# Kernel tuning notes

Measured on AMD Instinct MI355X. Metric: run time of the kernel, lower is better.

Reference implementation:

```python
import jax, jax.numpy as jnp
import numpy as np

MIN_VARIANCE = 0.1
W_MEAN = 1.0
W_DIST = 1.0
W_DISP = 1.0


def setup_inputs() -> dict:
    key = jax.random.key(0)
    k1, k2 = jax.random.split(key)
    cluster1 = jax.random.normal(k1, (8192, 128), dtype=jnp.float32)
    cluster2 = jax.random.normal(k2, (8192, 128), dtype=jnp.float32)
    return {"cluster1": cluster1, "cluster2": cluster2}


def _mean_loss(c1, c2):
    m1 = jnp.mean(c1, axis=0)
    m2 = jnp.mean(c2, axis=0)
    return jnp.mean((m1 - m2) ** 2)  # F.mse_loss default 'mean'


def _distance_loss(c1, c2):
    # min_j ||c1_i - c2_j||^2, fused via ||a||^2 - 2 a b^T + ||b||^2
    sq1 = jnp.sum(c1 * c1, axis=1)  # [N1]
    sq2 = jnp.sum(c2 * c2, axis=1)  # [N2]
    cross = c1 @ c2.T               # [N1, N2]
    d2 = sq1[:, None] - 2.0 * cross + sq2[None, :]
    return jnp.mean(jnp.min(d2, axis=1))


def _dispersion_loss(c, min_variance=MIN_VARIANCE):
    mean = jnp.mean(c, axis=0)
    variances = jnp.mean((c - mean) ** 2, axis=0)
    return jnp.mean(jax.nn.relu(min_variance - variances))


def reference(cluster1, cluster2):
    return (W_MEAN * _mean_loss(cluster1, cluster2)
            + W_DIST * _distance_loss(cluster1, cluster2)
            + W_DISP * _dispersion_loss(cluster1))
```

## Files before the change

kernel.cpp:

```cpp
#include <hip/hip_runtime.h>
#include <hip/hip_bf16.h>

#define N_ROWS 8192
#define DIMS   128

typedef __bf16 bf16x8 __attribute__((ext_vector_type(8)));
typedef float  f32x4  __attribute__((ext_vector_type(4)));

__device__ __forceinline__ unsigned enc_f32(float f) {
    int i = __float_as_int(f);
    return (unsigned)(i ^ ((i >> 31) | 0x80000000));
}
__device__ __forceinline__ float dec_f32(unsigned u) {
    int i = (u & 0x80000000u) ? (int)(u ^ 0x80000000u) : ~(int)u;
    return __int_as_float(i);
}

struct alignas(8) B4 { __hip_bfloat16 h0, h1, h2, h3; };

__global__ __launch_bounds__(256) void prep_k(const float* __restrict__ c1,
                                              const float* __restrict__ c2,
                                              __hip_bfloat16* __restrict__ c1b,
                                              __hip_bfloat16* __restrict__ c2b,
                                              float* __restrict__ sq1,
                                              float* __restrict__ sq2,
                                              float* __restrict__ part,
                                              unsigned* __restrict__ minrow) {
    const int tid  = threadIdx.x;
    const int lane = tid & 63;
    const int wave = tid >> 6;
    const int half = lane >> 5;
    const int l32  = lane & 31;
    const int cl   = blockIdx.x >> 7;
    const int blk  = blockIdx.x & 127;

    if (tid < 32) minrow[blockIdx.x * 32 + tid] = 0xFFFFFFFFu;

    const float* __restrict__ src    = cl ? c2 : c1;
    __hip_bfloat16* __restrict__ dst = cl ? c2b : c1b;
    float* __restrict__ sq           = cl ? sq2 : sq1;
    const float scale                = cl ? 1.0f : -2.0f;

    float4 cs = {0.f, 0.f, 0.f, 0.f};
    float4 cq = {0.f, 0.f, 0.f, 0.f};

    #pragma unroll 4
    for (int i = 0; i < 8; ++i) {
        const int row = blk * 64 + wave * 16 + i * 2 + half;
        float4 x = *reinterpret_cast<const float4*>(src + (size_t)row * DIMS + l32 * 4);
        B4 b4{__float2bfloat16(scale * x.x), __float2bfloat16(scale * x.y),
              __float2bfloat16(scale * x.z), __float2bfloat16(scale * x.w)};
        *reinterpret_cast<B4*>(dst + (size_t)row * DIMS + l32 * 4) = b4;
        float s = x.x * x.x + x.y * x.y + x.z * x.z + x.w * x.w;
        #pragma unroll
        for (int m = 16; m; m >>= 1) s += __shfl_xor(s, m);
        if (l32 == 0) sq[row] = s;
        cs.x += x.x; cs.y += x.y; cs.z += x.z; cs.w += x.w;
        cq.x += x.x * x.x; cq.y += x.y * x.y; cq.z += x.z * x.z; cq.w += x.w * x.w;
    }

    cs.x += __shfl_xor(cs.x, 32); cs.y += __shfl_xor(cs.y, 32);
    cs.z += __shfl_xor(cs.z, 32); cs.w += __shfl_xor(cs.w, 32);
    cq.x += __shfl_xor(cq.x, 32); cq.y += __shfl_xor(cq.y, 32);
    cq.z += __shfl_xor(cq.z, 32); cq.w += __shfl_xor(cq.w, 32);

    __shared__ float4 lds4[4][32];
    lds4[wave][l32] = cs;
    __syncthreads();
    if (tid < 32) {
        float4 a = lds4[0][tid], b = lds4[1][tid], c = lds4[2][tid], d = lds4[3][tid];
        float4 t = {a.x + b.x + c.x + d.x, a.y + b.y + c.y + d.y,
                    a.z + b.z + c.z + d.z, a.w + b.w + c.w + d.w};
        const int base = cl ? 32768 : 0;
        part[base + (4 * tid + 0) * 128 + blk] = t.x;
        part[base + (4 * tid + 1) * 128 + blk] = t.y;
        part[base + (4 * tid + 2) * 128 + blk] = t.z;
        part[base + (4 * tid + 3) * 128 + blk] = t.w;
    }
    __syncthreads();
    lds4[wave][l32] = cq;
    __syncthreads();
    if (tid < 32 && cl == 0) {
        float4 a = lds4[0][tid], b = lds4[1][tid], c = lds4[2][tid], d = lds4[3][tid];
        float4 t = {a.x + b.x + c.x + d.x, a.y + b.y + c.y + d.y,
                    a.z + b.z + c.z + d.z, a.w + b.w + c.w + d.w};
        part[16384 + (4 * tid + 0) * 128 + blk] = t.x;
        part[16384 + (4 * tid + 1) * 128 + blk] = t.y;
        part[16384 + (4 * tid + 2) * 128 + blk] = t.z;
        part[16384 + (4 * tid + 3) * 128 + blk] = t.w;
    }
}

__global__ __launch_bounds__(256, 2) void dist_k(const __hip_bfloat16* __restrict__ c1b,
                                                 const __hip_bfloat16* __restrict__ c2b,
                                                 const float* __restrict__ sq1,
                                                 const float* __restrict__ sq2,
                                                 unsigned* __restrict__ minrow) {
    const int lane = threadIdx.x & 63;
    const int wave = threadIdx.x >> 6;
    const int lo = lane & 15;
    const int hi = lane >> 4;
    const int rb = blockIdx.x >> 5;
    const int cb = blockIdx.x & 31;
    const int row0 = rb * 512 + wave * 128;
    const int col0 = cb * 256;

    uint4 a_u[8][4];
    #pragma unroll
    for (int rt = 0; rt < 8; ++rt)
        #pragma unroll
        for (int ks = 0; ks < 4; ++ks)
            a_u[rt][ks] = *reinterpret_cast<const uint4*>(
                c1b + (size_t)(row0 + rt * 16 + lo) * DIMS + ks * 32 + hi * 8);

    #pragma unroll
    for (int rt = 0; rt < 8; ++rt)
        #pragma unroll
        for (int ks = 0; ks < 4; ++ks)
            asm volatile("" : "+v"(a_u[rt][ks].x), "+v"(a_u[rt][ks].y),
                              "+v"(a_u[rt][ks].z), "+v"(a_u[rt][ks].w));

    float rmin[8][4];
    #pragma unroll
    for (int rt = 0; rt < 8; ++rt)
        #pragma unroll
        for (int r = 0; r < 4; ++r)
            rmin[rt][r] = __builtin_inff();

    bf16x8 bcur[4];
    float tcur;
    {
        const int J = col0 + lo;
        tcur = sq2[J];
        #pragma unroll
        for (int ks = 0; ks < 4; ++ks)
            bcur[ks] = *reinterpret_cast<const bf16x8*>(
                c2b + (size_t)J * DIMS + ks * 32 + hi * 8);
    }

    #pragma unroll 2
    for (int ct = 0; ct < 16; ++ct) {
        const int Jn = col0 + (((ct + 1) & 15) << 4) + lo;
        const float tnext = sq2[Jn];
        bf16x8 bnext[4];
        #pragma unroll
        for (int ks = 0; ks < 4; ++ks)
            bnext[ks] = *reinterpret_cast<const bf16x8*>(
                c2b + (size_t)Jn * DIMS + ks * 32 + hi * 8);

        __builtin_amdgcn_s_setprio(1);
        #pragma unroll
        for (int rt = 0; rt < 8; ++rt) {
            f32x4 acc = {tcur, tcur, tcur, tcur};
            #pragma unroll
            for (int ks = 0; ks < 4; ++ks)
                acc = __builtin_amdgcn_mfma_f32_16x16x32_bf16(
                    __builtin_bit_cast(bf16x8, a_u[rt][ks]), bcur[ks], acc, 0, 0, 0);
            #pragma unroll
            for (int r = 0; r < 4; ++r)
                rmin[rt][r] = fminf(rmin[rt][r], acc[r]);
        }
        __builtin_amdgcn_s_setprio(0);

        #pragma unroll
        for (int ks = 0; ks < 4; ++ks) bcur[ks] = bnext[ks];
        tcur = tnext;
    }

    #pragma unroll
    for (int rt = 0; rt < 8; ++rt)
        #pragma unroll
        for (int r = 0; r < 4; ++r) {
            float v = rmin[rt][r];
            v = fminf(v, __shfl_xor(v, 1));
            v = fminf(v, __shfl_xor(v, 2));
            v = fminf(v, __shfl_xor(v, 4));
            v = fminf(v, __shfl_xor(v, 8));
            rmin[rt][r] = v;
        }

    if (lo == 0) {
        #pragma unroll
        for (int rt = 0; rt < 8; ++rt)
            #pragma unroll
            for (int r = 0; r < 4; ++r) {
                int row = row0 + rt * 16 + hi * 4 + r;
                atomicMin(&minrow[row], enc_f32(rmin[rt][r] + sq1[row]));
            }
    }
}

__global__ __launch_bounds__(256) void final_k(const unsigned* __restrict__ minrow,
                                               const float* __restrict__ part,
                                               float* __restrict__ out) {
    __shared__ float red[256];
    __shared__ float cs[384];
    const int tid = threadIdx.x;

    for (int j = tid; j < 384; j += 256) {
        const float4* p = reinterpret_cast<const float4*>(part + j * 128);
        float4 a = {0.f, 0.f, 0.f, 0.f};
        #pragma unroll 8
        for (int b = 0; b < 32; ++b) {
            float4 v = p[b];
            a.x += v.x; a.y += v.y; a.z += v.z; a.w += v.w;
        }
        cs[j] = a.x + a.y + a.z + a.w;
    }

    const uint4* m4 = reinterpret_cast<const uint4*>(minrow);
    float s = 0.f;
    #pragma unroll 2
    for (int i = tid; i < N_ROWS / 4; i += 256) {
        uint4 u = m4[i];
        s += dec_f32(u.x) + dec_f32(u.y) + dec_f32(u.z) + dec_f32(u.w);
    }

    __syncthreads();
    float m = 0.f;
    if (tid < DIMS) {
        const float inv_n = 1.0f / N_ROWS;
        float m1 = cs[tid] * inv_n;
        float vq = cs[128 + tid] * inv_n;
        float m2 = cs[256 + tid] * inv_n;
        float d  = m1 - m2;
        float var = vq - m1 * m1;
        m = d * d + fmaxf(0.1f - var, 0.0f);
    }

    red[tid] = s * (1.0f / N_ROWS) + m * (1.0f / DIMS);
    __syncthreads();
    for (int off = 128; off; off >>= 1) {
        if (tid < off) red[tid] += red[tid + off];
        __syncthreads();
    }
    if (tid == 0) out[0] = red[0];
}

extern "C" void kernel_launch(void* const* d_in, const int* in_sizes, int n_in,
                              void* d_out, int out_size, void* d_ws, size_t ws_size,
                              hipStream_t stream) {
    (void)in_sizes; (void)n_in; (void)out_size; (void)ws_size;
    const float* c1 = (const float*)d_in[0];
    const float* c2 = (const float*)d_in[1];

    char* ws = (char*)d_ws;
    __hip_bfloat16* c1b = (__hip_bfloat16*)ws;
    __hip_bfloat16* c2b = (__hip_bfloat16*)(ws + (1u << 21));
    float* sq1          = (float*)(ws + (1u << 22));
    float* sq2          = sq1 + N_ROWS;
    unsigned* minrow    = (unsigned*)(sq2 + N_ROWS);
    float* part         = (float*)(minrow + N_ROWS);

    prep_k<<<256, 256, 0, stream>>>(c1, c2, c1b, c2b, sq1, sq2, part, minrow);
    dist_k<<<512, 256, 0, stream>>>(c1b, c2b, sq1, sq2, minrow);
    final_k<<<1, 256, 0, stream>>>(minrow, part, (float*)d_out);
}
```

Baseline: 51.61 us.

## Replace atomicMin row reduction with partial-min buffer and separate reduce kernel

Halves the rows per dist_k block (64 per wave instead of 128) and doubles the grid to 1024 blocks with launch bounds raised to 4 blocks per CU, to improve occupancy. Instead of encoded atomicMin into a per-row minimum, each block writes its partial minima to a [row, column-block] buffer, and a new reduce_k kernel takes the min over the 32 column blocks, adds sq1 and produces per-block sums. The software prefetch of B and the s_setprio hints are removed. In exchange it adds a kernel launch and extra global traffic for the partial-min buffer, and each A tile is now reused over fewer rows.

```diff
diff --git a/kernel.cpp b/kernel.cpp
--- a/kernel.cpp
+++ b/kernel.cpp
@@ -6,15 +6,6 @@
 
 typedef __bf16 bf16x8 __attribute__((ext_vector_type(8)));
 typedef float  f32x4  __attribute__((ext_vector_type(4)));
-
-__device__ __forceinline__ unsigned enc_f32(float f) {
-    int i = __float_as_int(f);
-    return (unsigned)(i ^ ((i >> 31) | 0x80000000));
-}
-__device__ __forceinline__ float dec_f32(unsigned u) {
-    int i = (u & 0x80000000u) ? (int)(u ^ 0x80000000u) : ~(int)u;
-    return __int_as_float(i);
-}
 
 struct alignas(8) B4 { __hip_bfloat16 h0, h1, h2, h3; };
 
@@ -24,8 +15,7 @@
                                               __hip_bfloat16* __restrict__ c2b,
                                               float* __restrict__ sq1,
                                               float* __restrict__ sq2,
-                                              float* __restrict__ part,
-                                              unsigned* __restrict__ minrow) {
+                                              float* __restrict__ part) {
     const int tid  = threadIdx.x;
     const int lane = tid & 63;
     const int wave = tid >> 6;
@@ -33,8 +23,6 @@
     const int l32  = lane & 31;
     const int cl   = blockIdx.x >> 7;
     const int blk  = blockIdx.x & 127;
-
-    if (tid < 32) minrow[blockIdx.x * 32 + tid] = 0xFFFFFFFFu;
 
     const float* __restrict__ src    = cl ? c2 : c1;
     __hip_bfloat16* __restrict__ dst = cl ? c2b : c1b;
@@ -91,84 +79,65 @@
     }
 }
 
-__global__ __launch_bounds__(256, 2) void dist_k(const __hip_bfloat16* __restrict__ c1b,
+__global__ __launch_bounds__(256, 4) void dist_k(const __hip_bfloat16* __restrict__ c1b,
                                                  const __hip_bfloat16* __restrict__ c2b,
-                                                 const float* __restrict__ sq1,
                                                  const float* __restrict__ sq2,
-                                                 unsigned* __restrict__ minrow) {
+                                                 float* __restrict__ pmin) {
     const int lane = threadIdx.x & 63;
     const int wave = threadIdx.x >> 6;
     const int lo = lane & 15;
     const int hi = lane >> 4;
     const int rb = blockIdx.x >> 5;
     const int cb = blockIdx.x & 31;
-    const int row0 = rb * 512 + wave * 128;
+    const int row0 = rb * 256 + wave * 64;
     const int col0 = cb * 256;
 
-    uint4 a_u[8][4];
-    #pragma unroll
-    for (int rt = 0; rt < 8; ++rt)
+    uint4 a_u[4][4];
+    #pragma unroll
+    for (int rt = 0; rt < 4; ++rt)
         #pragma unroll
         for (int ks = 0; ks < 4; ++ks)
             a_u[rt][ks] = *reinterpret_cast<const uint4*>(
                 c1b + (size_t)(row0 + rt * 16 + lo) * DIMS + ks * 32 + hi * 8);
 
     #pragma unroll
-    for (int rt = 0; rt < 8; ++rt)
+    for (int rt = 0; rt < 4; ++rt)
         #pragma unroll
         for (int ks = 0; ks < 4; ++ks)
             asm volatile("" : "+v"(a_u[rt][ks].x), "+v"(a_u[rt][ks].y),
                               "+v"(a_u[rt][ks].z), "+v"(a_u[rt][ks].w));
 
-    float rmin[8][4];
-    #pragma unroll
-    for (int rt = 0; rt < 8; ++rt)
+    float rmin[4][4];
+    #pragma unroll
+    for (int rt = 0; rt < 4; ++rt)
         #pragma unroll
         for (int r = 0; r < 4; ++r)
             rmin[rt][r] = __builtin_inff();
 
-    bf16x8 bcur[4];
-    float tcur;
-    {
-        const int J = col0 + lo;
-        tcur = sq2[J];
+    for (int ct = 0; ct < 16; ++ct) {
+        const int J = col0 + ct * 16 + lo;
+        const float t = sq2[J];
+        bf16x8 b[4];
         #pragma unroll
         for (int ks = 0; ks < 4; ++ks)
-            bcur[ks] = *reinterpret_cast<const bf16x8*>(
+            b[ks] = *reinterpret_cast<const bf16x8*>(
                 c2b + (size_t)J * DIMS + ks * 32 + hi * 8);
-    }
-
-    #pragma unroll 2
-    for (int ct = 0; ct < 16; ++ct) {
-        const int Jn = col0 + (((ct + 1) & 15) << 4) + lo;
-        const float tnext = sq2[Jn];
-        bf16x8 bnext[4];
-        #pragma unroll
-        for (int ks = 0; ks < 4; ++ks)
-            bnext[ks] = *reinterpret_cast<const bf16x8*>(
-                c2b + (size_t)Jn * DIMS + ks * 32 + hi * 8);
-
-        __builtin_amdgcn_s_setprio(1);
-        #pragma unroll
-        for (int rt = 0; rt < 8; ++rt) {
-            f32x4 acc = {tcur, tcur, tcur, tcur};
+
+        #pragma unroll
+        for (int rt = 0; rt < 4; ++rt) {
+            f32x4 acc = {t, t, t, t};
             #pragma unroll
             for (int ks = 0; ks < 4; ++ks)
                 acc = __builtin_amdgcn_mfma_f32_16x16x32_bf16(
-                    __builtin_bit_cast(bf16x8, a_u[rt][ks]), bcur[ks], acc, 0, 0, 0);
+                    __builtin_bit_cast(bf16x8, a_u[rt][ks]), b[ks], acc, 0, 0, 0);
             #pragma unroll
             for (int r = 0; r < 4; ++r)
                 rmin[rt][r] = fminf(rmin[rt][r], acc[r]);
         }
-        __builtin_amdgcn_s_setprio(0);
-
-        #pragma unroll
-        for (int ks = 0; ks < 4; ++ks) bcur[ks] = bnext[ks];
-        tcur = tnext;
-    }
-
-    #pragma unroll
-    for (int rt = 0; rt < 8; ++rt)
+    }
+
+    #pragma unroll
+    for (int rt = 0; rt < 4; ++rt)
         #pragma unroll
         for (int r = 0; r < 4; ++r) {
             float v = rmin[rt][r];
@@ -181,16 +150,42 @@
 
     if (lo == 0) {
         #pragma unroll
-        for (int rt = 0; rt < 8; ++rt)
+        for (int rt = 0; rt < 4; ++rt)
             #pragma unroll
             for (int r = 0; r < 4; ++r) {
                 int row = row0 + rt * 16 + hi * 4 + r;
-                atomicMin(&minrow[row], enc_f32(rmin[rt][r] + sq1[row]));
+                pmin[(size_t)row * 32 + cb] = rmin[rt][r];
             }
     }
 }
 
-__global__ __launch_bounds__(256) void final_k(const unsigned* __restrict__ minrow,
+__global__ __launch_bounds__(256) void reduce_k(const float* __restrict__ pmin,
+                                                const float* __restrict__ sq1,
+                                                float* __restrict__ rpart) {
+    __shared__ float red[256];
+    const int tid = threadIdx.x;
+    const int row = blockIdx.x * 256 + tid;
+
+    const float4* p = reinterpret_cast<const float4*>(pmin + (size_t)row * 32);
+    float4 m4 = p[0];
+    #pragma unroll
+    for (int i = 1; i < 8; ++i) {
+        float4 v = p[i];
+        m4.x = fminf(m4.x, v.x); m4.y = fminf(m4.y, v.y);
+        m4.z = fminf(m4.z, v.z); m4.w = fminf(m4.w, v.w);
+    }
+    float m = fminf(fminf(m4.x, m4.y), fminf(m4.z, m4.w)) + sq1[row];
+
+    red[tid] = m;
+    __syncthreads();
+    for (int off = 128; off; off >>= 1) {
+        if (tid < off) red[tid] += red[tid + off];
+        __syncthreads();
+    }
+    if (tid == 0) rpart[blockIdx.x] = red[0];
+}
+
+__global__ __launch_bounds__(256) void final_k(const float* __restrict__ rpart,
                                                const float* __restrict__ part,
                                                float* __restrict__ out) {
     __shared__ float red[256];
@@ -208,13 +203,7 @@
         cs[j] = a.x + a.y + a.z + a.w;
     }
 
-    const uint4* m4 = reinterpret_cast<const uint4*>(minrow);
-    float s = 0.f;
-    #pragma unroll 2
-    for (int i = tid; i < N_ROWS / 4; i += 256) {
-        uint4 u = m4[i];
-        s += dec_f32(u.x) + dec_f32(u.y) + dec_f32(u.z) + dec_f32(u.w);
-    }
+    float s = (tid < 32) ? rpart[tid] : 0.0f;
 
     __syncthreads();
     float m = 0.f;
@@ -249,10 +238,12 @@
     __hip_bfloat16* c2b = (__hip_bfloat16*)(ws + (1u << 21));
     float* sq1          = (float*)(ws + (1u << 22));
     float* sq2          = sq1 + N_ROWS;
-    unsigned* minrow    = (unsigned*)(sq2 + N_ROWS);
-    float* part         = (float*)(minrow + N_ROWS);
-
-    prep_k<<<256, 256, 0, stream>>>(c1, c2, c1b, c2b, sq1, sq2, part, minrow);
-    dist_k<<<512, 256, 0, stream>>>(c1b, c2b, sq1, sq2, minrow);
-    final_k<<<1, 256, 0, stream>>>(minrow, part, (float*)d_out);
-}
+    float* pmin         = sq2 + N_ROWS;
+    float* part         = pmin + (size_t)N_ROWS * 32;
+    float* rpart        = part + 3 * 16384;
+
+    prep_k<<<256, 256, 0, stream>>>(c1, c2, c1b, c2b, sq1, sq2, part);
+    dist_k<<<1024, 256, 0, stream>>>(c1b, c2b, sq2, pmin);
+    reduce_k<<<32, 256, 0, stream>>>(pmin, sq1, rpart);
+    final_k<<<1, 256, 0, stream>>>(rpart, part, (float*)d_out);
+}
```

Measured after the change: 67.15 us. +30.1%, slower.
